# Optimization experiments

Measured on AMD Instinct MI355X. Metric: run time of the kernel, lower is better.

The kernel has to match this reference:

```python
import jax, jax.numpy as jnp
import numpy as np

B, N, D, H = 2, 512, 256, 8
HD = D // H
DFF = 4 * D
EPS = 1e-5


def layer_norm(x, g, b):
    m = jnp.mean(x, axis=-1, keepdims=True)
    v = jnp.mean(jnp.square(x - m), axis=-1, keepdims=True)
    return (x - m) * jax.lax.rsqrt(v + EPS) * g + b


def setup_inputs() -> dict:
    key = jax.random.key(0)
    ks = jax.random.split(key, 16)
    s = 0.02
    return {
        "node_features": jax.random.normal(ks[0], (B, N, D), jnp.float32),
        "edge_features": jax.random.normal(ks[1], (B, N, N, D), jnp.float32),
        "adjacency_mask": jax.random.randint(ks[2], (B, N, N), 0, 2, jnp.int32),
        "node_norm_g": jnp.ones((D,), jnp.float32),
        "node_norm_b": jnp.zeros((D,), jnp.float32),
        "edge_norm_g": jnp.ones((D,), jnp.float32),
        "edge_norm_b": jnp.zeros((D,), jnp.float32),
        "Wq": jax.random.normal(ks[3], (D, D), jnp.float32) * s,
        "bq": jnp.zeros((D,), jnp.float32),
        "Wk": jax.random.normal(ks[4], (D, D), jnp.float32) * s,
        "bk": jnp.zeros((D,), jnp.float32),
        "Wv": jax.random.normal(ks[5], (D, D), jnp.float32) * s,
        "bv": jnp.zeros((D,), jnp.float32),
        "Wo": jax.random.normal(ks[6], (D, D), jnp.float32) * s,
        "bo": jnp.zeros((D,), jnp.float32),
        "We": jax.random.normal(ks[7], (D, H), jnp.float32) * s,
        "be": jnp.zeros((H,), jnp.float32),
        "ff_norm_g": jnp.ones((D,), jnp.float32),
        "ff_norm_b": jnp.zeros((D,), jnp.float32),
        "W1": jax.random.normal(ks[8], (D, DFF), jnp.float32) * s,
        "b1": jnp.zeros((DFF,), jnp.float32),
        "W2": jax.random.normal(ks[9], (DFF, D), jnp.float32) * s,
        "b2": jnp.zeros((D,), jnp.float32),
    }


def reference(node_features, edge_features, adjacency_mask,
              node_norm_g, node_norm_b, edge_norm_g, edge_norm_b,
              Wq, bq, Wk, bk, Wv, bv, Wo, bo, We, be,
              ff_norm_g, ff_norm_b, W1, b1, W2, b2):
    x = node_features
    nn_ = layer_norm(x, node_norm_g, node_norm_b)
    # project and split heads: (B, H, N, HD)
    q = (nn_ @ Wq + bq).reshape(B, N, H, HD).transpose(0, 2, 1, 3)
    k = (nn_ @ Wk + bk).reshape(B, N, H, HD).transpose(0, 2, 1, 3)
    v = (nn_ @ Wv + bv).reshape(B, N, H, HD).transpose(0, 2, 1, 3)
    scores = jnp.einsum('bhnd,bhmd->bhnm', q, k) / jnp.sqrt(jnp.float32(HD))
    # edge bias: LayerNorm over D then Linear(D->H), move H first
    eb = layer_norm(edge_features, edge_norm_g, edge_norm_b) @ We + be  # (B,N,N,H)
    scores = scores + eb.transpose(0, 3, 1, 2)
    scores = jnp.where(adjacency_mask[:, None, :, :] == 0, -jnp.inf, scores)
    attn = jax.nn.softmax(scores, axis=-1)
    out = jnp.einsum('bhnm,bhmd->bhnd', attn, v)
    out = out.transpose(0, 2, 1, 3).reshape(B, N, D) @ Wo + bo
    x = x + out
    # feedforward (dropout is identity at inference)
    h = layer_norm(x, ff_norm_g, ff_norm_b)
    h = jax.nn.gelu(h @ W1 + b1, approximate=False) @ W2 + b2
    return x + h
```

## Files before the change

### kernel.cpp

```cpp
#include <hip/hip_runtime.h>
#include <hip/hip_bf16.h>

typedef unsigned int uint;

constexpr float EPS_ = 1e-5f;

#define DEV __device__ __forceinline__

DEV float gelu_(float x){ return 0.5f*x*(1.f + erff(x*0.70710678118654752f)); }

__global__ __launch_bounds__(256) void k_setup(
    const float* __restrict__ g, const float* __restrict__ b,
    const float* __restrict__ We, const float* __restrict__ be,
    float* __restrict__ GW, float* __restrict__ A, float* __restrict__ C)
{
    const int d = threadIdx.x;
    __shared__ float redA[256*8];
    __shared__ float redC[256*8];
    float gd = g[d], bd = b[d];
    #pragma unroll
    for (int h = 0; h < 8; ++h) {
        float w = We[d*8+h];
        float gw = gd*w;
        GW[d*8+h] = gw;
        redA[d*8+h] = gw;
        redC[d*8+h] = bd*w;
    }
    __syncthreads();
    for (int s = 128; s >= 1; s >>= 1) {
        if (d < s) {
            #pragma unroll
            for (int h = 0; h < 8; ++h) {
                redA[d*8+h] += redA[(d+s)*8+h];
                redC[d*8+h] += redC[(d+s)*8+h];
            }
        }
        __syncthreads();
    }
    if (d < 8) {
        A[d] = redA[d];
        C[d] = redC[d] + be[d];
    }
}

__global__ __launch_bounds__(256) void k_qkv(
    const float* __restrict__ x,
    const float* __restrict__ g, const float* __restrict__ bta,
    const float* __restrict__ Wq, const float* __restrict__ bq,
    const float* __restrict__ Wk, const float* __restrict__ bk,
    const float* __restrict__ Wv, const float* __restrict__ bv,
    float* __restrict__ q, float* __restrict__ k, float* __restrict__ v)
{
    const int t = threadIdx.x;
    const int wid = t >> 6, l = t & 63;
    const int r0 = blockIdx.x << 1;
    __shared__ float sxT[256*2];
    if (wid < 2) {
        const int row = r0 + wid;
        const float4 xv4 = ((const float4*)x)[row*64 + l];
        float s  = xv4.x + xv4.y + xv4.z + xv4.w;
        float q2 = xv4.x*xv4.x + xv4.y*xv4.y + xv4.z*xv4.z + xv4.w*xv4.w;
        #pragma unroll
        for (int o = 32; o >= 1; o >>= 1) { s += __shfl_xor(s, o); q2 += __shfl_xor(q2, o); }
        const float m = s * (1.f/256.f);
        const float rinv = rsqrtf(q2*(1.f/256.f) - m*m + EPS_);
        const float4 g4 = ((const float4*)g)[l];
        const float4 b4 = ((const float4*)bta)[l];
        sxT[(4*l+0)*2 + wid] = (xv4.x - m)*rinv*g4.x + b4.x;
        sxT[(4*l+1)*2 + wid] = (xv4.y - m)*rinv*g4.y + b4.y;
        sxT[(4*l+2)*2 + wid] = (xv4.z - m)*rinv*g4.z + b4.z;
        sxT[(4*l+3)*2 + wid] = (xv4.w - m)*rinv*g4.w + b4.w;
    }
    __syncthreads();
    float aq0 = bq[t], ak0 = bk[t], av0 = bv[t];
    float aq1 = aq0, ak1 = ak0, av1 = av0;
    for (int d = 0; d < 256; d += 2) {
        const float4 s4 = *((const float4*)&sxT[d*2]);
        const float wqa = Wq[d*256 + t], wqb = Wq[(d+1)*256 + t];
        const float wka = Wk[d*256 + t], wkb = Wk[(d+1)*256 + t];
        const float wva = Wv[d*256 + t], wvb = Wv[(d+1)*256 + t];
        aq0 = fmaf(s4.x, wqa, aq0); aq0 = fmaf(s4.z, wqb, aq0);
        aq1 = fmaf(s4.y, wqa, aq1); aq1 = fmaf(s4.w, wqb, aq1);
        ak0 = fmaf(s4.x, wka, ak0); ak0 = fmaf(s4.z, wkb, ak0);
        ak1 = fmaf(s4.y, wka, ak1); ak1 = fmaf(s4.w, wkb, ak1);
        av0 = fmaf(s4.x, wva, av0); av0 = fmaf(s4.z, wvb, av0);
        av1 = fmaf(s4.y, wva, av1); av1 = fmaf(s4.w, wvb, av1);
    }
    q[(r0+0)*256 + t] = aq0; q[(r0+1)*256 + t] = aq1;
    k[(r0+0)*256 + t] = ak0; k[(r0+1)*256 + t] = ak1;
    v[(r0+0)*256 + t] = av0; v[(r0+1)*256 + t] = av1;
}

__global__ __launch_bounds__(256) void k_eattn(
    const float4* __restrict__ ep,
    const int*   __restrict__ msk,
    const float* __restrict__ GWg, const float* __restrict__ Avec, const float* __restrict__ Cvec,
    const float* __restrict__ qg, const float* __restrict__ kg, const float* __restrict__ vg,
    float* __restrict__ ao)
{
    __shared__ float slds[256*33];
    __shared__ float sb[8*512];
    __shared__ float sp[8*512];
    __shared__ float sqv[256];
    __shared__ float sden[8];
    const int t = threadIdx.x;
    const int bi = blockIdx.x;
    const int b = bi >> 9;
    sqv[t] = qg[(size_t)bi*256 + t] * 0.17677669529663687f;
    __syncthreads();

    for (int half = 0; half < 2; ++half) {
        const long long rowBase = ((long long)bi << 9) + (half << 8);
        float sum = 0.f, ssq = 0.f;
        float S[8] = {0.f,0.f,0.f,0.f,0.f,0.f,0.f,0.f};
        for (int c = 0; c < 8; ++c) {
            #pragma unroll
            for (int kk = 0; kk < 8; ++kk) {
                int l2 = (kk << 8) + t;
                int r = l2 >> 3, u = l2 & 7;
                float4 val = ep[(rowBase + r)*64 + (c << 3) + u];
                *((float4*)&slds[r*33 + (u << 2)]) = val;
            }
            __syncthreads();
            const float* srow = &slds[t*33];
            const int dbase = c << 5;
            #pragma unroll
            for (int j4 = 0; j4 < 8; ++j4) {
                const float4 e4 = *((const float4*)&srow[j4 << 2]);
                const int d0 = dbase + (j4 << 2);
                #pragma unroll
                for (int u = 0; u < 4; ++u) {
                    const float e = (u==0) ? e4.x : (u==1) ? e4.y : (u==2) ? e4.z : e4.w;
                    const float* gw = &GWg[(size_t)(d0 + u) << 3];
                    sum += e;
                    ssq = fmaf(e, e, ssq);
                    S[0] = fmaf(e, gw[0], S[0]); S[1] = fmaf(e, gw[1], S[1]);
                    S[2] = fmaf(e, gw[2], S[2]); S[3] = fmaf(e, gw[3], S[3]);
                    S[4] = fmaf(e, gw[4], S[4]); S[5] = fmaf(e, gw[5], S[5]);
                    S[6] = fmaf(e, gw[6], S[6]); S[7] = fmaf(e, gw[7], S[7]);
                }
            }
            __syncthreads();
        }
        const float m = sum * (1.f/256.f);
        const float rinv = rsqrtf(ssq*(1.f/256.f) - m*m + EPS_);
        const float mb = (msk[rowBase + t] == 0) ? -1e30f : 0.f;
        const int jrow = (half << 8) + t;
        #pragma unroll
        for (int h = 0; h < 8; ++h)
            sb[h*512 + jrow] = rinv * (S[h] - m * Avec[h]) + Cvec[h] + mb;
    }
    __syncthreads();

    const int h = t >> 5, l = t & 31;
    const float* kb = kg + ((size_t)b << 9)*256 + h*32;
    float4 qv[8];
    {
        const float4* qr = (const float4*)(sqv + h*32);
        #pragma unroll
        for (int w = 0; w < 8; ++w) qv[w] = qr[w];
    }
    float sc[16];
    float pmax = -3.0e38f;
    #pragma unroll
    for (int mi = 0; mi < 16; ++mi) {
        const int j = l + (mi << 5);
        const float4* kr = (const float4*)(kb + (size_t)j*256);
        float a = 0.f;
        #pragma unroll
        for (int w = 0; w < 8; ++w) {
            const float4 kv = kr[w];
            a += kv.x*qv[w].x + kv.y*qv[w].y + kv.z*qv[w].z + kv.w*qv[w].w;
        }
        float s0 = a + sb[h*512 + j];
        sc[mi] = s0;
        pmax = fmaxf(pmax, s0);
    }
    #pragma unroll
    for (int o = 16; o >= 1; o >>= 1) pmax = fmaxf(pmax, __shfl_xor(pmax, o));
    float psum = 0.f;
    #pragma unroll
    for (int mi = 0; mi < 16; ++mi) {
        float p = __expf(sc[mi] - pmax);
        sp[h*512 + l + (mi << 5)] = p;
        psum += p;
    }
    #pragma unroll
    for (int o = 16; o >= 1; o >>= 1) psum += __shfl_xor(psum, o);
    if (l == 0) sden[h] = psum;
    __syncthreads();

    const float* vb = vg + ((size_t)b << 9)*256 + t;
    const float4* spr4 = (const float4*)&sp[h*512];
    float a0 = 0.f, a1 = 0.f, a2 = 0.f, a3 = 0.f;
    for (int j4 = 0; j4 < 128; ++j4) {
        const float4 p4 = spr4[j4];
        const float* vj = vb + ((size_t)j4 << 2)*256;
        a0 = fmaf(p4.x, vj[0],   a0);
        a1 = fmaf(p4.y, vj[256], a1);
        a2 = fmaf(p4.z, vj[512], a2);
        a3 = fmaf(p4.w, vj[768], a3);
    }
    ao[(size_t)bi*256 + t] = (a0+a1+a2+a3) / sden[h];
}

__global__ __launch_bounds__(256) void k_proj(
    const float* __restrict__ at, const float* __restrict__ Wo,
    const float* __restrict__ bo, const float* __restrict__ x,
    float* __restrict__ x1)
{
    const int t = threadIdx.x;
    const int wid = t >> 6, l = t & 63;
    const int r0 = blockIdx.x << 1;
    __shared__ float saT[256*2];
    if (wid < 2) {
        const float4 a4 = ((const float4*)at)[(r0 + wid)*64 + l];
        saT[(4*l+0)*2 + wid] = a4.x;
        saT[(4*l+1)*2 + wid] = a4.y;
        saT[(4*l+2)*2 + wid] = a4.z;
        saT[(4*l+3)*2 + wid] = a4.w;
    }
    __syncthreads();
    float A0 = bo[t], A1 = A0;
    for (int d = 0; d < 256; d += 2) {
        const float4 s4 = *((const float4*)&saT[d*2]);
        const float wa = Wo[d*256 + t], wb = Wo[(d+1)*256 + t];
        A0 = fmaf(s4.x, wa, A0); A0 = fmaf(s4.z, wb, A0);
        A1 = fmaf(s4.y, wa, A1); A1 = fmaf(s4.w, wb, A1);
    }
    x1[(r0+0)*256 + t] = A0 + x[(r0+0)*256 + t];
    x1[(r0+1)*256 + t] = A1 + x[(r0+1)*256 + t];
}

__global__ __launch_bounds__(256) void k_ff(
    const float* __restrict__ x1, const float* __restrict__ g,
    const float* __restrict__ bb,
    const float* __restrict__ W1, const float* __restrict__ b1,
    const float* __restrict__ W2, const float* __restrict__ b2,
    float* __restrict__ out)
{
    const int t = threadIdx.x;
    const int wid = t >> 6, l = t & 63;
    const int r0 = blockIdx.x << 2;
    __shared__ float shT[256*4];
    __shared__ float sfT[1024*4];
    {
        const int row = r0 + wid;
        const float4 xv4 = ((const float4*)x1)[row*64 + l];
        float s  = xv4.x + xv4.y + xv4.z + xv4.w;
        float q2 = xv4.x*xv4.x + xv4.y*xv4.y + xv4.z*xv4.z + xv4.w*xv4.w;
        #pragma unroll
        for (int o = 32; o >= 1; o >>= 1) { s += __shfl_xor(s, o); q2 += __shfl_xor(q2, o); }
        const float m = s * (1.f/256.f);
        const float rinv = rsqrtf(q2*(1.f/256.f) - m*m + EPS_);
        const float4 g4 = ((const float4*)g)[l];
        const float4 b4 = ((const float4*)bb)[l];
        shT[(4*l+0)*4 + wid] = (xv4.x - m)*rinv*g4.x + b4.x;
        shT[(4*l+1)*4 + wid] = (xv4.y - m)*rinv*g4.y + b4.y;
        shT[(4*l+2)*4 + wid] = (xv4.z - m)*rinv*g4.z + b4.z;
        shT[(4*l+3)*4 + wid] = (xv4.w - m)*rinv*g4.w + b4.w;
    }
    __syncthreads();
    const float4 bc = ((const float4*)b1)[t];
    float4 Ac0 = make_float4(bc.x,bc.x,bc.x,bc.x);
    float4 Ac1 = make_float4(bc.y,bc.y,bc.y,bc.y);
    float4 Ac2 = make_float4(bc.z,bc.z,bc.z,bc.z);
    float4 Ac3 = make_float4(bc.w,bc.w,bc.w,bc.w);
    const float4* W14 = (const float4*)W1;
    for (int d = 0; d < 256; ++d) {
        const float4 s4 = *((const float4*)&shT[d*4]);
        const float4 w4 = W14[d*256 + t];
        Ac0.x = fmaf(s4.x, w4.x, Ac0.x); Ac0.y = fmaf(s4.y, w4.x, Ac0.y);
        Ac0.z = fmaf(s4.z, w4.x, Ac0.z); Ac0.w = fmaf(s4.w, w4.x, Ac0.w);
        Ac1.x = fmaf(s4.x, w4.y, Ac1.x); Ac1.y = fmaf(s4.y, w4.y, Ac1.y);
        Ac1.z = fmaf(s4.z, w4.y, Ac1.z); Ac1.w = fmaf(s4.w, w4.y, Ac1.w);
        Ac2.x = fmaf(s4.x, w4.z, Ac2.x); Ac2.y = fmaf(s4.y, w4.z, Ac2.y);
        Ac2.z = fmaf(s4.z, w4.z, Ac2.z); Ac2.w = fmaf(s4.w, w4.z, Ac2.w);
        Ac3.x = fmaf(s4.x, w4.w, Ac3.x); Ac3.y = fmaf(s4.y, w4.w, Ac3.y);
        Ac3.z = fmaf(s4.z, w4.w, Ac3.z); Ac3.w = fmaf(s4.w, w4.w, Ac3.w);
    }
    *((float4*)&sfT[(4*t+0)*4]) = make_float4(gelu_(Ac0.x), gelu_(Ac0.y), gelu_(Ac0.z), gelu_(Ac0.w));
    *((float4*)&sfT[(4*t+1)*4]) = make_float4(gelu_(Ac1.x), gelu_(Ac1.y), gelu_(Ac1.z), gelu_(Ac1.w));
    *((float4*)&sfT[(4*t+2)*4]) = make_float4(gelu_(Ac2.x), gelu_(Ac2.y), gelu_(Ac2.z), gelu_(Ac2.w));
    *((float4*)&sfT[(4*t+3)*4]) = make_float4(gelu_(Ac3.x), gelu_(Ac3.y), gelu_(Ac3.z), gelu_(Ac3.w));
    __syncthreads();
    const float b2v = b2[t];
    float4 AO = make_float4(b2v,b2v,b2v,b2v);
    for (int kk = 0; kk < 1024; ++kk) {
        const float4 s4 = *((const float4*)&sfT[kk*4]);
        const float w = W2[kk*256 + t];
        AO.x = fmaf(s4.x, w, AO.x); AO.y = fmaf(s4.y, w, AO.y);
        AO.z = fmaf(s4.z, w, AO.z); AO.w = fmaf(s4.w, w, AO.w);
    }
    out[(r0+0)*256 + t] = AO.x + x1[(r0+0)*256 + t];
    out[(r0+1)*256 + t] = AO.y + x1[(r0+1)*256 + t];
    out[(r0+2)*256 + t] = AO.z + x1[(r0+2)*256 + t];
    out[(r0+3)*256 + t] = AO.w + x1[(r0+3)*256 + t];
}

extern "C" void kernel_launch(void* const* d_in, const int* in_sizes, int n_in,
                              void* d_out, int out_size, void* d_ws, size_t ws_size,
                              hipStream_t stream) {
    const float* x   = (const float*)d_in[0];
    const float* ef  = (const float*)d_in[1];
    const int*   am  = (const int*)d_in[2];
    const float* ng  = (const float*)d_in[3];
    const float* nb  = (const float*)d_in[4];
    const float* eg  = (const float*)d_in[5];
    const float* ebb = (const float*)d_in[6];
    const float* Wq  = (const float*)d_in[7];
    const float* bq  = (const float*)d_in[8];
    const float* Wk  = (const float*)d_in[9];
    const float* bk  = (const float*)d_in[10];
    const float* Wv  = (const float*)d_in[11];
    const float* bv  = (const float*)d_in[12];
    const float* Wo  = (const float*)d_in[13];
    const float* bo  = (const float*)d_in[14];
    const float* We  = (const float*)d_in[15];
    const float* be  = (const float*)d_in[16];
    const float* fg  = (const float*)d_in[17];
    const float* fb  = (const float*)d_in[18];
    const float* W1  = (const float*)d_in[19];
    const float* b1  = (const float*)d_in[20];
    const float* W2  = (const float*)d_in[21];
    const float* b2  = (const float*)d_in[22];

    float* ws  = (float*)d_ws;
    float* GW  = ws;
    float* Av  = ws + 2048;
    float* Cv  = ws + 2064;
    float* q   = ws + 4096;
    float* k   = q  + 262144;
    float* v   = k  + 262144;
    float* ao  = v  + 262144;
    float* x1  = ao + 262144;

    hipLaunchKernelGGL(k_setup, dim3(1), dim3(256), 0, stream, eg, ebb, We, be, GW, Av, Cv);
    hipLaunchKernelGGL(k_qkv, dim3(512), dim3(256), 0, stream,
                       x, ng, nb, Wq, bq, Wk, bk, Wv, bv, q, k, v);
    hipLaunchKernelGGL(k_eattn, dim3(1024), dim3(256), 0, stream,
                       (const float4*)ef, am, GW, Av, Cv, q, k, v, ao);
    hipLaunchKernelGGL(k_proj, dim3(512), dim3(256), 0, stream, ao, Wo, bo, x, x1);
    hipLaunchKernelGGL(k_ff, dim3(256), dim3(256), 0, stream,
                       x1, fg, fb, W1, b1, W2, b2, (float*)d_out);
}
```

Before: 330.7 us.

## Stage K through LDS for QK scores, shrink edge tile, reuse score buffer for probabilities

The edge-feature staging tile shrinks from 32 to 16 columns per chunk, which lowers LDS use per block and may allow more blocks per CU. Q·K scores are now computed by staging K rows through shared memory in coalesced chunks, with each thread owning one key row and all 8 heads. Previously each lane did strided global float4 loads of K. The softmax then works in place on the score buffer, and the separate probability array is removed. This adds a second loop of 16 barriers per half and extra K traffic through LDS, so more synchronization is traded for coalesced loads and higher occupancy.

```diff
diff --git a/kernel.cpp b/kernel.cpp
--- a/kernel.cpp
+++ b/kernel.cpp
@@ -95,12 +95,11 @@
     const float4* __restrict__ ep,
     const int*   __restrict__ msk,
     const float* __restrict__ GWg, const float* __restrict__ Avec, const float* __restrict__ Cvec,
-    const float* __restrict__ qg, const float* __restrict__ kg, const float* __restrict__ vg,
+    const float* __restrict__ qg, const float4* __restrict__ kg4, const float* __restrict__ vg,
     float* __restrict__ ao)
 {
-    __shared__ float slds[256*33];
+    __shared__ float slds[256*20];
     __shared__ float sb[8*512];
-    __shared__ float sp[8*512];
     __shared__ float sqv[256];
     __shared__ float sden[8];
     const int t = threadIdx.x;
@@ -111,27 +110,28 @@
 
     for (int half = 0; half < 2; ++half) {
         const long long rowBase = ((long long)bi << 9) + (half << 8);
+        const int krow0 = (b << 9) + (half << 8);
         float sum = 0.f, ssq = 0.f;
-        float S[8] = {0.f,0.f,0.f,0.f,0.f,0.f,0.f,0.f};
-        for (int c = 0; c < 8; ++c) {
-            #pragma unroll
-            for (int kk = 0; kk < 8; ++kk) {
-                int l2 = (kk << 8) + t;
-                int r = l2 >> 3, u = l2 & 7;
-                float4 val = ep[(rowBase + r)*64 + (c << 3) + u];
-                *((float4*)&slds[r*33 + (u << 2)]) = val;
+        float S[8]  = {0.f,0.f,0.f,0.f,0.f,0.f,0.f,0.f};
+        float qk[8] = {0.f,0.f,0.f,0.f,0.f,0.f,0.f,0.f};
+
+        for (int c = 0; c < 16; ++c) {
+            #pragma unroll
+            for (int kk = 0; kk < 4; ++kk) {
+                const int l2 = (kk << 8) + t;
+                const int r = l2 >> 2, u = l2 & 3;
+                *((float4*)&slds[r*20 + (u << 2)]) = ep[(rowBase + r)*64 + (c << 2) + u];
             }
             __syncthreads();
-            const float* srow = &slds[t*33];
-            const int dbase = c << 5;
-            #pragma unroll
-            for (int j4 = 0; j4 < 8; ++j4) {
+            const float* srow = &slds[t*20];
+            const int d0 = c << 4;
+            #pragma unroll
+            for (int j4 = 0; j4 < 4; ++j4) {
                 const float4 e4 = *((const float4*)&srow[j4 << 2]);
-                const int d0 = dbase + (j4 << 2);
                 #pragma unroll
                 for (int u = 0; u < 4; ++u) {
                     const float e = (u==0) ? e4.x : (u==1) ? e4.y : (u==2) ? e4.z : e4.w;
-                    const float* gw = &GWg[(size_t)(d0 + u) << 3];
+                    const float* gw = &GWg[(size_t)(d0 + (j4 << 2) + u) << 3];
                     sum += e;
                     ssq = fmaf(e, e, ssq);
                     S[0] = fmaf(e, gw[0], S[0]); S[1] = fmaf(e, gw[1], S[1]);
@@ -142,66 +142,80 @@
             }
             __syncthreads();
         }
+
+        for (int c = 0; c < 16; ++c) {
+            #pragma unroll
+            for (int kk = 0; kk < 4; ++kk) {
+                const int l2 = (kk << 8) + t;
+                const int r = l2 >> 2, u = l2 & 3;
+                *((float4*)&slds[r*20 + (u << 2)]) = kg4[(size_t)(krow0 + r)*64 + (c << 2) + u];
+            }
+            __syncthreads();
+            const float* srow = &slds[t*20];
+            const float4* q4p = (const float4*)&sqv[c << 4];
+            float acc = qk[c >> 1];
+            #pragma unroll
+            for (int j4 = 0; j4 < 4; ++j4) {
+                const float4 k4 = *((const float4*)&srow[j4 << 2]);
+                const float4 q4 = q4p[j4];
+                acc = fmaf(k4.x, q4.x, acc); acc = fmaf(k4.y, q4.y, acc);
+                acc = fmaf(k4.z, q4.z, acc); acc = fmaf(k4.w, q4.w, acc);
+            }
+            qk[c >> 1] = acc;
+            __syncthreads();
+        }
+
         const float m = sum * (1.f/256.f);
         const float rinv = rsqrtf(ssq*(1.f/256.f) - m*m + EPS_);
         const float mb = (msk[rowBase + t] == 0) ? -1e30f : 0.f;
         const int jrow = (half << 8) + t;
         #pragma unroll
         for (int h = 0; h < 8; ++h)
-            sb[h*512 + jrow] = rinv * (S[h] - m * Avec[h]) + Cvec[h] + mb;
-    }
-    __syncthreads();
-
-    const int h = t >> 5, l = t & 31;
-    const float* kb = kg + ((size_t)b << 9)*256 + h*32;
-    float4 qv[8];
+            sb[h*512 + jrow] = qk[h] + rinv * (S[h] - m * Avec[h]) + Cvec[h] + mb;
+    }
+    __syncthreads();
+
     {
-        const float4* qr = (const float4*)(sqv + h*32);
-        #pragma unroll
-        for (int w = 0; w < 8; ++w) qv[w] = qr[w];
-    }
-    float sc[16];
-    float pmax = -3.0e38f;
-    #pragma unroll
-    for (int mi = 0; mi < 16; ++mi) {
-        const int j = l + (mi << 5);
-        const float4* kr = (const float4*)(kb + (size_t)j*256);
-        float a = 0.f;
-        #pragma unroll
-        for (int w = 0; w < 8; ++w) {
-            const float4 kv = kr[w];
-            a += kv.x*qv[w].x + kv.y*qv[w].y + kv.z*qv[w].z + kv.w*qv[w].w;
-        }
-        float s0 = a + sb[h*512 + j];
-        sc[mi] = s0;
-        pmax = fmaxf(pmax, s0);
-    }
-    #pragma unroll
-    for (int o = 16; o >= 1; o >>= 1) pmax = fmaxf(pmax, __shfl_xor(pmax, o));
-    float psum = 0.f;
-    #pragma unroll
-    for (int mi = 0; mi < 16; ++mi) {
-        float p = __expf(sc[mi] - pmax);
-        sp[h*512 + l + (mi << 5)] = p;
-        psum += p;
-    }
-    #pragma unroll
-    for (int o = 16; o >= 1; o >>= 1) psum += __shfl_xor(psum, o);
-    if (l == 0) sden[h] = psum;
-    __syncthreads();
-
-    const float* vb = vg + ((size_t)b << 9)*256 + t;
-    const float4* spr4 = (const float4*)&sp[h*512];
-    float a0 = 0.f, a1 = 0.f, a2 = 0.f, a3 = 0.f;
-    for (int j4 = 0; j4 < 128; ++j4) {
-        const float4 p4 = spr4[j4];
-        const float* vj = vb + ((size_t)j4 << 2)*256;
-        a0 = fmaf(p4.x, vj[0],   a0);
-        a1 = fmaf(p4.y, vj[256], a1);
-        a2 = fmaf(p4.z, vj[512], a2);
-        a3 = fmaf(p4.w, vj[768], a3);
-    }
-    ao[(size_t)bi*256 + t] = (a0+a1+a2+a3) / sden[h];
+        const int h = t >> 5, l = t & 31;
+        float* base = &sb[h*512 + (l << 4)];
+        float4 s4[4];
+        float pmax = -3.0e38f;
+        #pragma unroll
+        for (int i = 0; i < 4; ++i) {
+            s4[i] = *((const float4*)&base[i << 2]);
+            pmax = fmaxf(pmax, fmaxf(fmaxf(s4[i].x, s4[i].y), fmaxf(s4[i].z, s4[i].w)));
+        }
+        #pragma unroll
+        for (int o = 16; o >= 1; o >>= 1) pmax = fmaxf(pmax, __shfl_xor(pmax, o));
+        float psum = 0.f;
+        #pragma unroll
+        for (int i = 0; i < 4; ++i) {
+            const float p0 = __expf(s4[i].x - pmax), p1 = __expf(s4[i].y - pmax);
+            const float p2 = __expf(s4[i].z - pmax), p3 = __expf(s4[i].w - pmax);
+            psum += (p0 + p1) + (p2 + p3);
+            *((float4*)&base[i << 2]) = make_float4(p0, p1, p2, p3);
+        }
+        #pragma unroll
+        for (int o = 16; o >= 1; o >>= 1) psum += __shfl_xor(psum, o);
+        if (l == 0) sden[h] = psum;
+    }
+    __syncthreads();
+
+    {
+        const int h = t >> 5;
+        const float* vb = vg + ((size_t)b << 9)*256 + t;
+        const float4* spr4 = (const float4*)&sb[h*512];
+        float a0 = 0.f, a1 = 0.f, a2 = 0.f, a3 = 0.f;
+        for (int j4 = 0; j4 < 128; ++j4) {
+            const float4 p4 = spr4[j4];
+            const float* vj = vb + ((size_t)j4 << 2)*256;
+            a0 = fmaf(p4.x, vj[0],   a0);
+            a1 = fmaf(p4.y, vj[256], a1);
+            a2 = fmaf(p4.z, vj[512], a2);
+            a3 = fmaf(p4.w, vj[768], a3);
+        }
+        ao[(size_t)bi*256 + t] = (a0+a1+a2+a3) / sden[h];
+    }
 }
 
 __global__ __launch_bounds__(256) void k_proj(
@@ -339,7 +353,7 @@
     hipLaunchKernelGGL(k_qkv, dim3(512), dim3(256), 0, stream,
                        x, ng, nb, Wq, bq, Wk, bk, Wv, bv, q, k, v);
     hipLaunchKernelGGL(k_eattn, dim3(1024), dim3(256), 0, stream,
-                       (const float4*)ef, am, GW, Av, Cv, q, k, v, ao);
+                       (const float4*)ef, am, GW, Av, Cv, q, (const float4*)k, v, ao);
     hipLaunchKernelGGL(k_proj, dim3(512), dim3(256), 0, stream, ao, Wo, bo, x, x1);
     hipLaunchKernelGGL(k_ff, dim3(256), dim3(256), 0, stream,
                        x1, fg, fb, W1, b1, W2, b2, (float*)d_out);
```

New measurement: 293.0 us. 1.13x faster.
